# Kernel optimization log

Hardware: AMD Instinct MI355X
Metric: run time of the kernel (lower is better)

Reference implementation:

```python
import jax, jax.numpy as jnp
import numpy as np

B, LQ, LK, E, HID, H = 4, 1024, 2048, 512, 512, 8


def _ln(x, g, b, eps=1e-5):
    mu = jnp.mean(x, -1, keepdims=True)
    var = jnp.mean((x - mu) ** 2, -1, keepdims=True)
    return (x - mu) * jax.lax.rsqrt(var + eps) * g + b


def _mha(q_in, k_in, v_in, Wq, bq, Wk, bk, Wv, bv, Wo, bo, nheads, q_valid, k_valid):
    # torch nn.MultiheadAttention (batch_first, eval/dropout=0) math
    Bq, Lq, Em = q_in.shape
    Lk = k_in.shape[1]
    hd = Em // nheads
    q = (q_in @ Wq.T + bq).reshape(Bq, Lq, nheads, hd)
    k = (k_in @ Wk.T + bk).reshape(Bq, Lk, nheads, hd)
    v = (v_in @ Wv.T + bv).reshape(Bq, Lk, nheads, hd)
    scale = 1.0 / np.sqrt(hd).astype(np.float32)
    s = jnp.einsum('bqhd,bkhd->bhqk', q, k) * scale
    if k_valid is not None:
        # valid query rows may only attend to valid key columns
        s = jnp.where(k_valid[:, None, None, :], s, jnp.finfo(s.dtype).min)
    w = jax.nn.softmax(s, axis=-1)
    # rows beyond a sample's length are fully masked in the torch nested path
    # (softmax -> NaN, later nan_to_num'd to 0); we zero them directly.
    w = jnp.where(q_valid[:, None, :, None], w, 0.0)
    o = jnp.einsum('bhqk,bkhd->bqhd', w, v).reshape(Bq, Lq, Em)
    return o @ Wo.T + bo, jnp.mean(w, axis=1)  # weights averaged over heads


def setup_inputs() -> dict:
    key = jax.random.key(0)
    ks = jax.random.split(key, 32)
    p = lambda i, shape: 0.02 * jax.random.normal(ks[i], shape, dtype=jnp.float32)
    inp = {
        'queries': jax.random.normal(ks[0], (B, LQ, E), dtype=jnp.float32),
        'keys': jax.random.normal(ks[1], (B, LK, E), dtype=jnp.float32),
        'q_len': jax.random.randint(ks[2], (B,), 1, LQ + 1),
        # cross-attention params
        'cWq': p(3, (E, E)), 'cbq': jnp.zeros((E,)),
        'cWk': p(4, (E, E)), 'cbk': jnp.zeros((E,)),
        'cWv': p(5, (E, E)), 'cbv': jnp.zeros((E,)),
        'cWo': p(6, (E, E)), 'cbo': jnp.zeros((E,)),
        # self-attention params
        'sWq': p(7, (HID, HID)), 'sbq': jnp.zeros((HID,)),
        'sWk': p(8, (HID, HID)), 'sbk': jnp.zeros((HID,)),
        'sWv': p(9, (HID, HID)), 'sbv': jnp.zeros((HID,)),
        'sWo': p(10, (HID, HID)), 'sbo': jnp.zeros((HID,)),
        # ffn + norms
        'Wf': p(11, (HID, E)), 'bf': jnp.zeros((HID,)),
        'g_cross': jnp.ones((E,)), 'b_cross': jnp.zeros((E,)),
        'g_ffn': jnp.ones((HID,)), 'b_ffn': jnp.zeros((HID,)),
        'g_self': jnp.ones((HID,)), 'b_self': jnp.zeros((HID,)),
    }
    return inp


def reference(queries, keys, q_len,
              cWq, cbq, cWk, cbk, cWv, cbv, cWo, cbo,
              sWq, sbq, sWk, sbk, sWv, sbv, sWo, sbo,
              Wf, bf, g_cross, b_cross, g_ffn, b_ffn, g_self, b_self):
    valid = jnp.arange(LQ)[None, :] < q_len[:, None]  # [B, LQ] ragged lengths
    q = jnp.where(valid[..., None], queries, 0.0)     # nested -> padded with 0
    # cross attention: valid rows attend to ALL keys (per the nested mask)
    cross, weights = _mha(q, keys, keys, cWq, cbq, cWk, cbk, cWv, cbv, cWo, cbo,
                          H, valid, None)
    q = _ln(jax.nn.silu(cross + q), g_cross, b_cross)
    f = q @ Wf.T + bf
    q = _ln(jax.nn.silu(q + f), g_ffn, b_ffn)  # q_dim == hidden_dim branch
    q = jnp.where(valid[..., None], q, 0.0)    # torch.nan_to_num on padded rows
    # self attention: valid rows attend only to valid rows of the same sample
    so, _ = _mha(q, q, q, sWq, sbq, sWk, sbk, sWv, sbv, sWo, sbo, H, valid, valid)
    q = _ln(jax.nn.silu(q + so), g_self, b_self)
    q = jnp.where(valid[..., None], q, 0.0)    # padded rows discarded by unbind
    return q, weights
```

## Files before the change

kernel.cpp:

```cpp
#include <hip/hip_runtime.h>

#define BB 4
#define SLQ 1024
#define SLK 2048
#define EE 512
#define HH 8
#define HD 64

typedef unsigned short u16;
typedef __attribute__((ext_vector_type(8))) short s16x8;
typedef __attribute__((ext_vector_type(4))) float f32x4;

__device__ __forceinline__ float bf2f(u16 u) {
  union { unsigned int i; float f; } v; v.i = ((unsigned int)u) << 16; return v.f;
}
__device__ __forceinline__ u16 f2bf(float f) {
  union { float f; unsigned int i; } v; v.f = f;
  unsigned int i = v.i;
  return (u16)((i + 0x7fffu + ((i >> 16) & 1u)) >> 16);
}

__device__ __forceinline__ void async16(const u16* g, u16* l) {
  __builtin_amdgcn_global_load_lds(
      (const __attribute__((address_space(1))) unsigned int*)g,
      (__attribute__((address_space(3))) unsigned int*)l, 16, 0, 0);
}

template<int BM, int BN, int MODE, int SKIPQ>
__global__ __launch_bounds__(256, (BM == 128 ? 4 : 6))
void gemm_nt(const u16* __restrict__ A, const u16* __restrict__ Bm,
             const float* __restrict__ bias, u16* __restrict__ C,
             int M, int N, int K, int lda, int ldb, int ldc,
             long sAz, long sBz, long sCz, float alpha, int Lsub,
             const int* __restrict__ qlen)
{
  constexpr int WTM = BM / 2, WTN = BN / 2;
  constexpr int MI = WTM / 16, NI = WTN / 16;
  constexpr int EPAD = WTN + 8;
  constexpr int SM1 = (BM + BN) * 32;
  constexpr int SM2 = (MODE == 0) ? 4 * WTM * EPAD : 0;
  constexpr int SM = (SM1 > SM2) ? SM1 : SM2;

  const int z = blockIdx.z;
  const int tileM = blockIdx.y * BM;
  const int tileN = blockIdx.x * BN;

  if (SKIPQ == 1) { if (tileM >= qlen[z >> 3]) return; }
  if (SKIPQ == 2) { int b = tileM >> 10; if ((tileM & 1023) >= qlen[b]) return; }

  __shared__ __align__(16) u16 smem[SM];
  u16* ldsA = smem;
  u16* ldsB = smem + BM * 32;

  const int t = threadIdx.x;
  const int lane = t & 63;
  const int wave = t >> 6;
  const int waveM = wave >> 1;
  const int waveN = wave & 1;
  const int lm = lane & 15;
  const int kg = lane >> 4;

  const u16* Ab = A + (long)z * sAz + (long)tileM * lda;
  const u16* Bb = Bm + (long)z * sBz + (long)tileN * ldb;

  f32x4 acc[MI][NI];
#pragma unroll
  for (int i = 0; i < MI; ++i)
#pragma unroll
    for (int j = 0; j < NI; ++j) acc[i][j] = (f32x4){0.f, 0.f, 0.f, 0.f};

  for (int kt = 0; kt < K; kt += 32) {
    __syncthreads();
#pragma unroll
    for (int i = 0; i < (BM * 4) / 256; ++i) {
      int c = i * 256 + t;
      async16(Ab + (long)(c >> 2) * lda + kt + (c & 3) * 8, ldsA + (c - lane) * 8);
    }
#pragma unroll
    for (int i = 0; i < (BN * 4) / 256; ++i) {
      int c = i * 256 + t;
      async16(Bb + (long)(c >> 2) * ldb + kt + (c & 3) * 8, ldsB + (c - lane) * 8);
    }
    __syncthreads();

    s16x8 aF[MI], bF[NI];
#pragma unroll
    for (int i = 0; i < MI; ++i)
      aF[i] = *(const s16x8*)&ldsA[(waveM * WTM + i * 16 + lm) * 32 + kg * 8];
#pragma unroll
    for (int j = 0; j < NI; ++j)
      bF[j] = *(const s16x8*)&ldsB[(waveN * WTN + j * 16 + lm) * 32 + kg * 8];
#pragma unroll
    for (int i = 0; i < MI; ++i)
#pragma unroll
      for (int j = 0; j < NI; ++j)
        acc[i][j] = __builtin_amdgcn_mfma_f32_16x16x32_bf16(aF[i], bF[j], acc[i][j], 0, 0, 0);
  }

  if (MODE == 0) {
    u16* ep = smem + wave * (WTM * EPAD);
    __syncthreads();
#pragma unroll
    for (int i = 0; i < MI; ++i)
#pragma unroll
      for (int j = 0; j < NI; ++j) {
        int n = waveN * WTN + j * 16 + lm;
        float bv = bias ? bias[tileN + n] : 0.0f;
#pragma unroll
        for (int r = 0; r < 4; ++r)
          ep[(i * 16 + kg * 4 + r) * EPAD + j * 16 + lm] = f2bf(acc[i][j][r] * alpha + bv);
      }
    const long Crow = (long)z * sCz + (long)(tileM + waveM * WTM) * ldc + tileN + waveN * WTN;
#pragma unroll
    for (int it = 0; it < (WTM * WTN) / 512; ++it) {
      int idx = it * 64 + lane;
      int row = idx / (WTN / 8), seg = idx % (WTN / 8);
      *(uint4*)&C[Crow + (long)row * ldc + seg * 8] =
          *(const uint4*)&ep[row * EPAD + seg * 8];
    }
  } else {
#pragma unroll
    for (int j = 0; j < NI; ++j) {
      int n = tileN + waveN * WTN + j * 16 + lm;
      float bv = bias ? bias[n] : 0.0f;
#pragma unroll
      for (int i = 0; i < MI; ++i) {
#pragma unroll
        for (int r = 0; r < 4; ++r) {
          int m = tileM + waveM * WTM + i * 16 + kg * 4 + r;
          float v = acc[i][j][r] * alpha + bv;
          int b = m / Lsub, l = m - b * Lsub;
          int h = n >> 6, d = n & 63;
          C[(((long)(b * HH + h) * Lsub + l) << 6) + d] = f2bf(v);
        }
      }
    }
  }
}

template<int BM, int BN, int SKIPQ, int NPROJ>
__global__ __launch_bounds__(256, 6)
void gemm_proj(const u16* __restrict__ A,
               const u16* B0, const u16* B1, const u16* B2,
               const float* bias0, const float* bias1, const float* bias2,
               u16* C0, u16* C1, u16* C2,
               int M, int lda, int Lsub, const int* __restrict__ qlen)
{
  constexpr int WTM = BM / 2, WTN = BN / 2;
  constexpr int MI = WTM / 16, NI = WTN / 16;

  const int z = blockIdx.z;
  const int tileM = blockIdx.y * BM;
  const int tileN = blockIdx.x * BN;
  if (SKIPQ == 2) { int b = tileM >> 10; if ((tileM & 1023) >= qlen[b]) return; }

  const u16* Bm = (z == 0) ? B0 : (z == 1) ? B1 : B2;
  const float* bias = (z == 0) ? bias0 : (z == 1) ? bias1 : bias2;
  u16* C = (z == 0) ? C0 : (z == 1) ? C1 : C2;
  const bool tr = (z == NPROJ - 1);

  __shared__ __align__(16) u16 smem[(BM + BN) * 32];
  u16* ldsA = smem;
  u16* ldsB = smem + BM * 32;

  const int t = threadIdx.x;
  const int lane = t & 63;
  const int wave = t >> 6;
  const int waveM = wave >> 1;
  const int waveN = wave & 1;
  const int lm = lane & 15;
  const int kg = lane >> 4;

  const u16* Ab = A + (long)tileM * lda;
  const u16* Bb = Bm + (long)tileN * EE;

  f32x4 acc[MI][NI];
#pragma unroll
  for (int i = 0; i < MI; ++i)
#pragma unroll
    for (int j = 0; j < NI; ++j) acc[i][j] = (f32x4){0.f, 0.f, 0.f, 0.f};

  for (int kt = 0; kt < EE; kt += 32) {
    __syncthreads();
#pragma unroll
    for (int i = 0; i < (BM * 4) / 256; ++i) {
      int c = i * 256 + t;
      async16(Ab + (long)(c >> 2) * lda + kt + (c & 3) * 8, ldsA + (c - lane) * 8);
    }
#pragma unroll
    for (int i = 0; i < (BN * 4) / 256; ++i) {
      int c = i * 256 + t;
      async16(Bb + (long)(c >> 2) * EE + kt + (c & 3) * 8, ldsB + (c - lane) * 8);
    }
    __syncthreads();

    s16x8 aF[MI], bF[NI];
#pragma unroll
    for (int i = 0; i < MI; ++i)
      aF[i] = *(const s16x8*)&ldsA[(waveM * WTM + i * 16 + lm) * 32 + kg * 8];
#pragma unroll
    for (int j = 0; j < NI; ++j)
      bF[j] = *(const s16x8*)&ldsB[(waveN * WTN + j * 16 + lm) * 32 + kg * 8];
#pragma unroll
    for (int i = 0; i < MI; ++i)
#pragma unroll
      for (int j = 0; j < NI; ++j)
        acc[i][j] = __builtin_amdgcn_mfma_f32_16x16x32_bf16(aF[i], bF[j], acc[i][j], 0, 0, 0);
  }

  if (!tr) {
#pragma unroll
    for (int j = 0; j < NI; ++j) {
      int n = tileN + waveN * WTN + j * 16 + lm;
      float bv = bias[n];
#pragma unroll
      for (int i = 0; i < MI; ++i)
#pragma unroll
        for (int r = 0; r < 4; ++r) {
          int m = tileM + waveM * WTM + i * 16 + kg * 4 + r;
          int b = m / Lsub, l = m - b * Lsub;
          int h = n >> 6, d = n & 63;
          C[(((long)(b * HH + h) * Lsub + l) << 6) + d] = f2bf(acc[i][j][r] + bv);
        }
    }
  } else {
    constexpr int PAD = BM + 8;
    const int bb = tileM / Lsub;
    const int l0 = tileM - bb * Lsub;
#pragma unroll
    for (int c = 0; c < BN / 32; ++c) {
      __syncthreads();
#pragma unroll
      for (int j = 0; j < NI; ++j) {
        int nloc = waveN * WTN + j * 16 + lm;
        if (nloc >= c * 32 && nloc < c * 32 + 32) {
          int nl = nloc - c * 32;
          float bv = bias[tileN + nloc];
#pragma unroll
          for (int i = 0; i < MI; ++i)
#pragma unroll
            for (int r = 0; r < 4; ++r) {
              int mm = waveM * WTM + i * 16 + kg * 4 + r;
              smem[nl * PAD + mm] = f2bf(acc[i][j][r] + bv);
            }
        }
      }
      __syncthreads();
#pragma unroll
      for (int v = 0; v < (32 * BM) / (256 * 8); ++v) {
        int idx = v * 256 + t;
        int nl = idx / (BM / 8), m8 = idx % (BM / 8);
        int n = tileN + c * 32 + nl;
        int h = n >> 6, d = n & 63;
        *(uint4*)&C[((long)(bb * HH + h) * HD + d) * Lsub + l0 + m8 * 8] =
            *(const uint4*)&smem[nl * PAD + m8 * 8];
      }
    }
  }
}

__global__ __launch_bounds__(256, 3)
void cross_flash_chunk(const u16* __restrict__ Qc, const u16* __restrict__ Kc,
                       const u16* __restrict__ Vt, u16* __restrict__ Opart,
                       float2* __restrict__ ml, const int* __restrict__ qlen)
{
  const int qt = blockIdx.x;
  const int bh = blockIdx.y;
  const int ck = blockIdx.z;
  const int b = bh >> 3;
  if (qt * 64 >= qlen[b]) return;

  __shared__ __align__(16) u16 Kt[128 * 72];
  __shared__ __align__(16) u16 Vl[64 * 136];
  __shared__ __align__(16) u16 Pl[4 * 16 * 136];

  const int t = threadIdx.x, lane = t & 63, w = t >> 6;
  const int col = lane & 15, quad = lane >> 4;

  const u16* Qb = Qc + (long)bh * SLQ * HD;
  const u16* Kb = Kc + (long)bh * SLK * HD;
  const u16* Vb = Vt + (long)bh * HD * SLK;

  s16x8 aQ[2];
#pragma unroll
  for (int kk = 0; kk < 2; ++kk)
    aQ[kk] = *(const s16x8*)(Qb + (long)(qt * 64 + w * 16 + col) * HD + kk * 32 + quad * 8);

  f32x4 O[4];
  float mr[4], lr[4];
#pragma unroll
  for (int n = 0; n < 4; ++n) O[n] = (f32x4){0.f, 0.f, 0.f, 0.f};
#pragma unroll
  for (int r = 0; r < 4; ++r) { mr[r] = -1e30f; lr[r] = 0.f; }

  u16* Pw = Pl + w * 16 * 136;

  for (int kt = 0; kt < 4; ++kt) {
    const int k0 = ck * 512 + kt * 128;
    __syncthreads();
    for (int c = t; c < 1024; c += 256) {
      int r = c >> 3, c8 = c & 7;
      *(uint4*)&Kt[r * 72 + c8 * 8] = *(const uint4*)(Kb + (long)(k0 + r) * HD + c8 * 8);
    }
    for (int c = t; c < 1024; c += 256) {
      int d = c >> 4, c16 = c & 15;
      *(uint4*)&Vl[d * 136 + c16 * 8] = *(const uint4*)(Vb + (long)d * SLK + k0 + c16 * 8);
    }
    __syncthreads();

    f32x4 s[8];
#pragma unroll
    for (int j = 0; j < 8; ++j) s[j] = (f32x4){0.f, 0.f, 0.f, 0.f};
#pragma unroll
    for (int j = 0; j < 8; ++j)
#pragma unroll
      for (int kk = 0; kk < 2; ++kk) {
        s16x8 bK = *(const s16x8*)&Kt[(j * 16 + col) * 72 + kk * 32 + quad * 8];
        s[j] = __builtin_amdgcn_mfma_f32_16x16x32_bf16(aQ[kk], bK, s[j], 0, 0, 0);
      }
#pragma unroll
    for (int j = 0; j < 8; ++j)
#pragma unroll
      for (int r = 0; r < 4; ++r)
        s[j][r] *= 0.125f;
#pragma unroll
    for (int r = 0; r < 4; ++r) {
      float tm = s[0][r];
#pragma unroll
      for (int j = 1; j < 8; ++j) tm = fmaxf(tm, s[j][r]);
#pragma unroll
      for (int o = 1; o <= 8; o <<= 1) tm = fmaxf(tm, __shfl_xor(tm, o));
      float mnew = fmaxf(mr[r], tm);
      float alpha = __expf(mr[r] - mnew);
      mr[r] = mnew;
      float ps = 0.f;
#pragma unroll
      for (int j = 0; j < 8; ++j) {
        float p = __expf(s[j][r] - mnew);
        s[j][r] = p;
        ps += p;
      }
#pragma unroll
      for (int o = 1; o <= 8; o <<= 1) ps += __shfl_xor(ps, o);
      lr[r] = lr[r] * alpha + ps;
#pragma unroll
      for (int n = 0; n < 4; ++n) O[n][r] *= alpha;
    }
#pragma unroll
    for (int j = 0; j < 8; ++j)
#pragma unroll
      for (int r = 0; r < 4; ++r)
        Pw[(quad * 4 + r) * 136 + j * 16 + col] = f2bf(s[j][r]);
#pragma unroll
    for (int kk = 0; kk < 4; ++kk) {
      s16x8 aP = *(const s16x8*)&Pw[col * 136 + kk * 32 + quad * 8];
#pragma unroll
      for (int n = 0; n < 4; ++n) {
        s16x8 bV = *(const s16x8*)&Vl[(n * 16 + col) * 136 + kk * 32 + quad * 8];
        O[n] = __builtin_amdgcn_mfma_f32_16x16x32_bf16(aP, bV, O[n], 0, 0, 0);
      }
    }
  }

#pragma unroll
  for (int r = 0; r < 4; ++r) {
    int q = qt * 64 + w * 16 + quad * 4 + r;
    long gq = (long)bh * SLQ + q;
#pragma unroll
    for (int n = 0; n < 4; ++n)
      Opart[(gq * 4 + ck) * 64 + n * 16 + col] = f2bf(O[n][r]);
    if (col == 0) ml[gq * 4 + ck] = (float2){mr[r], lr[r]};
  }
}

__global__ __launch_bounds__(256)
void cross_combine(const u16* __restrict__ Opart, const float2* __restrict__ ml,
                   u16* __restrict__ attn, float2* __restrict__ stat,
                   const int* __restrict__ qlen)
{
  int gr = blockIdx.x * 16 + (threadIdx.x >> 4);
  int bh = gr >> 10, q = gr & 1023;
  int b = bh >> 3, h = bh & 7;
  if (q >= qlen[b]) return;
  int d = (threadIdx.x & 15) * 4;
  long base = (long)gr * 4;
  float M = -1e30f;
#pragma unroll
  for (int c = 0; c < 4; ++c) M = fmaxf(M, ml[base + c].x);
  float L = 0.f;
  float ax = 0.f, ay = 0.f, az = 0.f, aw = 0.f;
#pragma unroll
  for (int c = 0; c < 4; ++c) {
    float2 st = ml[base + c];
    float wgt = __expf(st.x - M);
    L += st.y * wgt;
    const u16* p = Opart + (base + c) * 64 + d;
    ax += bf2f(p[0]) * wgt; ay += bf2f(p[1]) * wgt;
    az += bf2f(p[2]) * wgt; aw += bf2f(p[3]) * wgt;
  }
  if (d == 0) stat[gr] = (float2){M, L};
  float inv = 1.0f / L;
  unsigned int lo = (unsigned int)f2bf(ax * inv) | ((unsigned int)f2bf(ay * inv) << 16);
  unsigned int hi = (unsigned int)f2bf(az * inv) | ((unsigned int)f2bf(aw * inv) << 16);
  *(uint2*)&attn[((long)b * SLQ + q) * EE + h * HD + d] = (uint2){lo, hi};
}

__global__ __launch_bounds__(256, 4)
void wmean_recompute(const u16* __restrict__ Qc, const u16* __restrict__ Kc,
                     const float2* __restrict__ stat, float* __restrict__ outw,
                     const int* __restrict__ qlen)
{
  const int kt = blockIdx.x;
  const int qt = blockIdx.y;
  const int b  = blockIdx.z;
  const int qn = qlen[b];
  const int q0 = qt * 64;
  const int t = threadIdx.x, lane = t & 63, w = t >> 6;
  const int col = lane & 15, quad = lane >> 4;

  float* wr = outw + ((long)b * SLQ + q0) * SLK + kt * 128;

  if (q0 >= qn) {
    float4 z = {0.f, 0.f, 0.f, 0.f};
    for (int i = t; i < 64 * 32; i += 256) {
      int row = i >> 5, c = (i & 31) << 2;
      *(float4*)&wr[(long)row * SLK + c] = z;
    }
    return;
  }

  __shared__ __align__(16) u16 Kl[128 * 72];

  const int qw = q0 + w * 16;
  const u16* Kbase = Kc + ((long)b * HH * SLK + (long)kt * 128) * HD;

  uint4 kreg[4];
#pragma unroll
  for (int i = 0; i < 4; ++i) {
    int c = i * 256 + t;
    kreg[i] = *(const uint4*)(Kbase + (long)(c >> 3) * HD + (c & 7) * 8);
  }

  f32x4 acc[8];
#pragma unroll
  for (int j = 0; j < 8; ++j) acc[j] = (f32x4){0.f, 0.f, 0.f, 0.f};

#pragma unroll 1
  for (int h = 0; h < 8; ++h) {
    const int bh = b * 8 + h;
    __syncthreads();
#pragma unroll
    for (int i = 0; i < 4; ++i) {
      int c = i * 256 + t;
      *(uint4*)&Kl[(c >> 3) * 72 + (c & 7) * 8] = kreg[i];
    }
    if (h < 7) {
      const u16* Kn = Kbase + (long)(h + 1) * SLK * HD;
#pragma unroll
      for (int i = 0; i < 4; ++i) {
        int c = i * 256 + t;
        kreg[i] = *(const uint4*)(Kn + (long)(c >> 3) * HD + (c & 7) * 8);
      }
    }
    const u16* Qb = Qc + ((long)bh * SLQ + qw) * HD;
    s16x8 aQ0 = *(const s16x8*)(Qb + col * HD + quad * 8);
    s16x8 aQ1 = *(const s16x8*)(Qb + col * HD + 32 + quad * 8);
    float m_[4], il_[4];
#pragma unroll
    for (int r = 0; r < 4; ++r) {
      float2 st = stat[(long)bh * SLQ + qw + quad * 4 + r];
      m_[r] = st.x; il_[r] = 0.125f / st.y;
    }
    __syncthreads();

    f32x4 s[8];
#pragma unroll
    for (int j = 0; j < 8; ++j) s[j] = (f32x4){0.f, 0.f, 0.f, 0.f};
#pragma unroll
    for (int j = 0; j < 8; ++j) {
      s16x8 bK0 = *(const s16x8*)&Kl[(j * 16 + col) * 72 + quad * 8];
      s16x8 bK1 = *(const s16x8*)&Kl[(j * 16 + col) * 72 + 32 + quad * 8];
      s[j] = __builtin_amdgcn_mfma_f32_16x16x32_bf16(aQ0, bK0, s[j], 0, 0, 0);
      s[j] = __builtin_amdgcn_mfma_f32_16x16x32_bf16(aQ1, bK1, s[j], 0, 0, 0);
    }
#pragma unroll
    for (int j = 0; j < 8; ++j)
#pragma unroll
      for (int r = 0; r < 4; ++r)
        acc[j][r] += __expf(s[j][r] * 0.125f - m_[r]) * il_[r];
  }

#pragma unroll
  for (int r = 0; r < 4; ++r) {
    int row = w * 16 + quad * 4 + r;
    bool v = (q0 + row) < qn;
#pragma unroll
    for (int j = 0; j < 8; ++j)
      wr[(long)row * SLK + j * 16 + col] = v ? acc[j][r] : 0.f;
  }
}

__global__ __launch_bounds__(256, 3)
void self_flash_chunk(const u16* __restrict__ Qc, const u16* __restrict__ Kc,
                      const u16* __restrict__ Vt, u16* __restrict__ Opart,
                      float2* __restrict__ ml, const int* __restrict__ qlen)
{
  const int qt = blockIdx.x;
  const int bh = blockIdx.y;
  const int ck = blockIdx.z;
  const int b = bh >> 3;
  const int kmax = qlen[b];
  if (qt * 64 >= kmax || ck * 256 >= kmax) return;

  __shared__ __align__(16) u16 Kt[128 * 72];
  __shared__ __align__(16) u16 Vl[64 * 136];
  __shared__ __align__(16) u16 Pl[4 * 16 * 136];

  const int t = threadIdx.x, lane = t & 63, w = t >> 6;
  const int col = lane & 15, quad = lane >> 4;

  const u16* Qb = Qc + (long)bh * SLQ * HD;
  const u16* Kb = Kc + (long)bh * SLQ * HD;
  const u16* Vb = Vt + (long)bh * HD * SLQ;

  s16x8 aQ[2];
#pragma unroll
  for (int kk = 0; kk < 2; ++kk)
    aQ[kk] = *(const s16x8*)(Qb + (long)(qt * 64 + w * 16 + col) * HD + kk * 32 + quad * 8);

  f32x4 O[4];
  float mr[4], lr[4];
#pragma unroll
  for (int n = 0; n < 4; ++n) O[n] = (f32x4){0.f, 0.f, 0.f, 0.f};
#pragma unroll
  for (int r = 0; r < 4; ++r) { mr[r] = -1e30f; lr[r] = 0.f; }

  u16* Pw = Pl + w * 16 * 136;

  for (int kt = 0; kt < 2; ++kt) {
    const int k0 = ck * 256 + kt * 128;
    if (k0 >= kmax) break;
    __syncthreads();
    for (int c = t; c < 1024; c += 256) {
      int r = c >> 3, c8 = c & 7;
      *(uint4*)&Kt[r * 72 + c8 * 8] = *(const uint4*)(Kb + (long)(k0 + r) * HD + c8 * 8);
    }
    for (int c = t; c < 1024; c += 256) {
      int d = c >> 4, c16 = c & 15;
      *(uint4*)&Vl[d * 136 + c16 * 8] = *(const uint4*)(Vb + (long)d * SLQ + k0 + c16 * 8);
    }
    __syncthreads();

    f32x4 s[8];
#pragma unroll
    for (int j = 0; j < 8; ++j) s[j] = (f32x4){0.f, 0.f, 0.f, 0.f};
#pragma unroll
    for (int j = 0; j < 8; ++j)
#pragma unroll
      for (int kk = 0; kk < 2; ++kk) {
        s16x8 bK = *(const s16x8*)&Kt[(j * 16 + col) * 72 + kk * 32 + quad * 8];
        s[j] = __builtin_amdgcn_mfma_f32_16x16x32_bf16(aQ[kk], bK, s[j], 0, 0, 0);
      }
#pragma unroll
    for (int j = 0; j < 8; ++j) {
      bool ok = (k0 + j * 16 + col) < kmax;
#pragma unroll
      for (int r = 0; r < 4; ++r)
        s[j][r] = ok ? s[j][r] * 0.125f : -1e30f;
    }
#pragma unroll
    for (int r = 0; r < 4; ++r) {
      float tm = s[0][r];
#pragma unroll
      for (int j = 1; j < 8; ++j) tm = fmaxf(tm, s[j][r]);
#pragma unroll
      for (int o = 1; o <= 8; o <<= 1) tm = fmaxf(tm, __shfl_xor(tm, o));
      float mnew = fmaxf(mr[r], tm);
      float alpha = __expf(mr[r] - mnew);
      mr[r] = mnew;
      float ps = 0.f;
#pragma unroll
      for (int j = 0; j < 8; ++j) {
        float p = __expf(s[j][r] - mnew);
        s[j][r] = p;
        ps += p;
      }
#pragma unroll
      for (int o = 1; o <= 8; o <<= 1) ps += __shfl_xor(ps, o);
      lr[r] = lr[r] * alpha + ps;
#pragma unroll
      for (int n = 0; n < 4; ++n) O[n][r] *= alpha;
    }
#pragma unroll
    for (int j = 0; j < 8; ++j)
#pragma unroll
      for (int r = 0; r < 4; ++r)
        Pw[(quad * 4 + r) * 136 + j * 16 + col] = f2bf(s[j][r]);
#pragma unroll
    for (int kk = 0; kk < 4; ++kk) {
      s16x8 aP = *(const s16x8*)&Pw[col * 136 + kk * 32 + quad * 8];
#pragma unroll
      for (int n = 0; n < 4; ++n) {
        s16x8 bV = *(const s16x8*)&Vl[(n * 16 + col) * 136 + kk * 32 + quad * 8];
        O[n] = __builtin_amdgcn_mfma_f32_16x16x32_bf16(aP, bV, O[n], 0, 0, 0);
      }
    }
  }

#pragma unroll
  for (int r = 0; r < 4; ++r) {
    int q = qt * 64 + w * 16 + quad * 4 + r;
    long gq = (long)bh * SLQ + q;
#pragma unroll
    for (int n = 0; n < 4; ++n)
      Opart[(gq * 4 + ck) * 64 + n * 16 + col] = f2bf(O[n][r]);
    if (col == 0) ml[gq * 4 + ck] = (float2){mr[r], lr[r]};
  }
}

__global__ __launch_bounds__(256)
void self_combine(const u16* __restrict__ Opart, const float2* __restrict__ ml,
                  u16* __restrict__ attn, const int* __restrict__ qlen)
{
  int gr = blockIdx.x * 16 + (threadIdx.x >> 4);
  int bh = gr >> 10, q = gr & 1023;
  int b = bh >> 3, h = bh & 7;
  int kmax = qlen[b];
  if (q >= kmax) return;
  int NC = (kmax + 255) >> 8;
  int d = (threadIdx.x & 15) * 4;
  long base = (long)gr * 4;
  float M = -1e30f;
  for (int c = 0; c < NC; ++c) M = fmaxf(M, ml[base + c].x);
  float L = 0.f;
  float ax = 0.f, ay = 0.f, az = 0.f, aw = 0.f;
  for (int c = 0; c < NC; ++c) {
    float2 st = ml[base + c];
    float wgt = __expf(st.x - M);
    L += st.y * wgt;
    const u16* p = Opart + (base + c) * 64 + d;
    ax += bf2f(p[0]) * wgt; ay += bf2f(p[1]) * wgt;
    az += bf2f(p[2]) * wgt; aw += bf2f(p[3]) * wgt;
  }
  float inv = 1.0f / L;
  unsigned int lo = (unsigned int)f2bf(ax * inv) | ((unsigned int)f2bf(ay * inv) << 16);
  unsigned int hi = (unsigned int)f2bf(az * inv) | ((unsigned int)f2bf(aw * inv) << 16);
  *(uint2*)&attn[((long)b * SLQ + q) * EE + h * HD + d] = (uint2){lo, hi};
}

__global__ __launch_bounds__(256)
void cvt_all(const float* __restrict__ queries, const float* __restrict__ keys,
             const int* __restrict__ qlen,
             const float* w0, const float* w1, const float* w2, const float* w3,
             const float* w4, const float* w5, const float* w6, const float* w7,
             const float* w8,
             u16* __restrict__ q0, u16* __restrict__ keysb, u16* __restrict__ Wb) {
  int blk = blockIdx.x;
  int t = threadIdx.x;
  const float* src;
  u16* dst;
  long off;
  bool mask = false;
  int b = 0, q = 0;
  if (blk < 1024) {
    off = (long)blk * 2048 + t * 8;
    int row = (int)(off >> 9);
    b = row >> 10; q = row & 1023;
    mask = true;
    src = queries; dst = q0;
  } else if (blk < 3072) {
    off = (long)(blk - 1024) * 2048 + t * 8;
    src = keys; dst = keysb;
  } else {
    int mat = (blk - 3072) >> 7, part = (blk - 3072) & 127;
    const float* srcs[9] = {w0, w1, w2, w3, w4, w5, w6, w7, w8};
    src = srcs[mat];
    off = (long)part * 2048 + t * 8;
    dst = Wb + (long)mat * EE * EE;
  }
  s16x8 o = (s16x8){0, 0, 0, 0, 0, 0, 0, 0};
  if (!mask || q < qlen[b]) {
    float4 a = *(const float4*)&src[off];
    float4 c = *(const float4*)&src[off + 4];
    o[0] = (short)f2bf(a.x); o[1] = (short)f2bf(a.y);
    o[2] = (short)f2bf(a.z); o[3] = (short)f2bf(a.w);
    o[4] = (short)f2bf(c.x); o[5] = (short)f2bf(c.y);
    o[6] = (short)f2bf(c.z); o[7] = (short)f2bf(c.w);
  }
  *(s16x8*)&dst[off] = o;
}

__device__ __forceinline__ float blockSum(float v, float* red4) {
#pragma unroll
  for (int o = 32; o; o >>= 1) v += __shfl_xor(v, o);
  if ((threadIdx.x & 63) == 0) red4[threadIdx.x >> 6] = v;
  __syncthreads();
  v = red4[0] + red4[1] + red4[2] + red4[3];
  __syncthreads();
  return v;
}

template<int OUTF32>
__global__ __launch_bounds__(256)
void silu_ln_kernel(const u16* __restrict__ x1, const u16* __restrict__ x2,
                    const float* __restrict__ g, const float* __restrict__ beta,
                    const int* __restrict__ qlen, void* __restrict__ outv, int mode) {
  int row = blockIdx.x;
  int b = row >> 10, q = row & 1023;
  int t = threadIdx.x;
  if (mode && q >= qlen[b]) {
    if (mode == 1) {
      if (OUTF32) {
        float* o = (float*)outv + (long)row * EE;
        o[2 * t] = 0.f; o[2 * t + 1] = 0.f;
      } else {
        u16* o = (u16*)outv + (long)row * EE;
        *(unsigned int*)&o[2 * t] = 0u;
      }
    }
    return;
  }
  __shared__ float red4[4];
  const u16* p1 = x1 + (long)row * EE;
  const u16* p2 = x2 + (long)row * EE;
  float a0 = bf2f(p1[2 * t]) + bf2f(p2[2 * t]);
  float a1 = bf2f(p1[2 * t + 1]) + bf2f(p2[2 * t + 1]);
  a0 = a0 / (1.f + __expf(-a0));
  a1 = a1 / (1.f + __expf(-a1));
  float mu = blockSum(a0 + a1, red4) * (1.f / 512.f);
  float d0 = a0 - mu, d1 = a1 - mu;
  float var = blockSum(d0 * d0 + d1 * d1, red4) * (1.f / 512.f);
  float rs = rsqrtf(var + 1e-5f);
  float r0 = d0 * rs * g[2 * t] + beta[2 * t];
  float r1 = d1 * rs * g[2 * t + 1] + beta[2 * t + 1];
  if (OUTF32) {
    float* o = (float*)outv + (long)row * EE;
    o[2 * t] = r0; o[2 * t + 1] = r1;
  } else {
    u16* o = (u16*)outv + (long)row * EE;
    o[2 * t] = f2bf(r0); o[2 * t + 1] = f2bf(r1);
  }
}

extern "C" void kernel_launch(void* const* d_in, const int* in_sizes, int n_in,
                              void* d_out, int out_size, void* d_ws, size_t ws_size,
                              hipStream_t stream) {
  const float* queries = (const float*)d_in[0];
  const float* keys    = (const float*)d_in[1];
  const int*   qlen    = (const int*)d_in[2];
  const float* cWq = (const float*)d_in[3],  *cbq = (const float*)d_in[4];
  const float* cWk = (const float*)d_in[5],  *cbk = (const float*)d_in[6];
  const float* cWv = (const float*)d_in[7],  *cbv = (const float*)d_in[8];
  const float* cWo = (const float*)d_in[9],  *cbo = (const float*)d_in[10];
  const float* sWq = (const float*)d_in[11], *sbq = (const float*)d_in[12];
  const float* sWk = (const float*)d_in[13], *sbk = (const float*)d_in[14];
  const float* sWv = (const float*)d_in[15], *sbv = (const float*)d_in[16];
  const float* sWo = (const float*)d_in[17], *sbo = (const float*)d_in[18];
  const float* Wf  = (const float*)d_in[19], *bfb = (const float*)d_in[20];
  const float* g_cross = (const float*)d_in[21], *b_cross = (const float*)d_in[22];
  const float* g_ffn   = (const float*)d_in[23], *b_ffn   = (const float*)d_in[24];
  const float* g_self  = (const float*)d_in[25], *b_self  = (const float*)d_in[26];

  float* out_q = (float*)d_out;
  float* out_w = out_q + (long)BB * SLQ * EE;

  u16* ws = (u16*)d_ws;
  u16* S     = ws;
  u16* Qc    = S   + (long)BB * HH * SLQ * SLK;
  u16* Kc    = Qc  + (long)BB * HH * SLQ * HD;
  u16* Vt    = Kc  + (long)BB * HH * SLK * HD;
  u16* q0    = Vt  + (long)BB * HH * SLK * HD;
  u16* keysb = q0  + (long)BB * SLQ * EE;
  u16* attn  = keysb + (long)BB * SLK * EE;
  u16* proj  = attn + (long)BB * SLQ * EE;
  u16* q1    = proj + (long)BB * SLQ * EE;
  u16* fbuf  = q1  + (long)BB * SLQ * EE;
  u16* q2    = fbuf + (long)BB * SLQ * EE;
  u16* Wb    = q2  + (long)BB * SLQ * EE;
  const long WSLOT = (long)EE * EE;
  u16*    Cpb  = Wb + 9 * WSLOT;
  float2* stat = (float2*)(Cpb + 8388608);

  float2* mlC = (float2*)(S + 33554432);

  u16*    OpS = S;
  float2* mlS = (float2*)(S + 8388608);

  u16* bWq = Wb + 0 * WSLOT; u16* bWk = Wb + 1 * WSLOT; u16* bWv = Wb + 2 * WSLOT;
  u16* bWo = Wb + 3 * WSLOT; u16* bsWq = Wb + 4 * WSLOT; u16* bsWk = Wb + 5 * WSLOT;
  u16* bsWv = Wb + 6 * WSLOT; u16* bsWo = Wb + 7 * WSLOT; u16* bWf = Wb + 8 * WSLOT;

  dim3 blk(256);
  const int MQ = BB * SLQ;
  const int MK = BB * SLK;

  cvt_all<<<dim3(3072 + 9 * 128), blk, 0, stream>>>(
      queries, keys, qlen, cWq, cWk, cWv, cWo, sWq, sWk, sWv, sWo, Wf, q0, keysb, Wb);

  gemm_nt<64, 64, 1, 2><<<dim3(EE / 64, MQ / 64, 1), blk, 0, stream>>>(
      q0, bWq, cbq, Qc, MQ, EE, EE, EE, EE, 0, 0, 0, 0, 1.0f, SLQ, qlen);
  gemm_proj<64, 64, 0, 2><<<dim3(EE / 64, MK / 64, 2), blk, 0, stream>>>(
      keysb, bWk, bWv, nullptr, cbk, cbv, nullptr, Kc, Vt, nullptr, MK, EE, SLK, qlen);

  cross_flash_chunk<<<dim3(16, 32, 4), blk, 0, stream>>>(Qc, Kc, Vt, Cpb, mlC, qlen);
  cross_combine<<<dim3(2048), blk, 0, stream>>>(Cpb, mlC, attn, stat, qlen);
  wmean_recompute<<<dim3(16, 16, BB), blk, 0, stream>>>(Qc, Kc, stat, out_w, qlen);

  gemm_nt<64, 64, 0, 2><<<dim3(EE / 64, MQ / 64, 1), blk, 0, stream>>>(
      attn, bWo, cbo, proj, MQ, EE, EE, EE, EE, EE, 0, 0, 0, 1.0f, SLQ, qlen);

  silu_ln_kernel<0><<<dim3(MQ), blk, 0, stream>>>(proj, q0, g_cross, b_cross, qlen, q1, 2);

  gemm_nt<64, 64, 0, 2><<<dim3(EE / 64, MQ / 64, 1), blk, 0, stream>>>(
      q1, bWf, bfb, fbuf, MQ, EE, EE, EE, EE, EE, 0, 0, 0, 1.0f, SLQ, qlen);

  silu_ln_kernel<0><<<dim3(MQ), blk, 0, stream>>>(q1, fbuf, g_ffn, b_ffn, qlen, q2, 1);

  gemm_proj<64, 64, 2, 3><<<dim3(EE / 64, MQ / 64, 3), blk, 0, stream>>>(
      q2, bsWq, bsWk, bsWv, sbq, sbk, sbv, Qc, Kc, Vt, MQ, EE, SLQ, qlen);

  self_flash_chunk<<<dim3(16, 32, 4), blk, 0, stream>>>(Qc, Kc, Vt, OpS, mlS, qlen);
  self_combine<<<dim3(2048), blk, 0, stream>>>(OpS, mlS, attn, qlen);

  gemm_nt<64, 64, 0, 2><<<dim3(EE / 64, MQ / 64, 1), blk, 0, stream>>>(
      attn, bsWo, sbo, proj, MQ, EE, EE, EE, EE, EE, 0, 0, 0, 1.0f, SLQ, qlen);

  silu_ln_kernel<1><<<dim3(MQ), blk, 0, stream>>>(q2, proj, g_self, b_self, qlen, out_q, 1);
}
```

Before: 358.6 us.

## Prefetch next K/V tile into registers and remap flash blocks across XCDs

Both flash-attention chunk kernels now load the next 128-key K and V tile into registers while the current tile is being computed, then write it to shared memory at the start of the next iteration. This is meant to hide global memory latency behind the MFMA and softmax work. The 3D grid is also flattened to 1D with a block-index swizzle (lin&7 selects a group of 256), so that neighbouring work lands on the same XCD for L2 reuse. The cost is extra VGPRs for the eight uint4 staging registers, which may hurt occupancy at launch bounds of 3 blocks per CU.

New measurement: 380.4 us. 6.1% more time.

```diff
diff --git a/kernel.cpp b/kernel.cpp
--- a/kernel.cpp
+++ b/kernel.cpp
@@ -264,9 +264,11 @@
                        const u16* __restrict__ Vt, u16* __restrict__ Opart,
                        float2* __restrict__ ml, const int* __restrict__ qlen)
 {
-  const int qt = blockIdx.x;
-  const int bh = blockIdx.y;
-  const int ck = blockIdx.z;
+  const int lin = blockIdx.x;
+  const int lid = (lin & 7) * 256 + (lin >> 3);
+  const int qt = lid & 15;
+  const int bh = (lid >> 4) & 31;
+  const int ck = lid >> 9;
   const int b = bh >> 3;
   if (qt * 64 >= qlen[b]) return;
 
@@ -295,16 +297,45 @@
 
   u16* Pw = Pl + w * 16 * 136;
 
+  uint4 kreg[4], vreg[4];
+  {
+    const int k0 = ck * 512;
+#pragma unroll
+    for (int i = 0; i < 4; ++i) {
+      int c = i * 256 + t;
+      kreg[i] = *(const uint4*)(Kb + (long)(k0 + (c >> 3)) * HD + (c & 7) * 8);
+    }
+#pragma unroll
+    for (int i = 0; i < 4; ++i) {
+      int c = i * 256 + t;
+      vreg[i] = *(const uint4*)(Vb + (long)(c >> 4) * SLK + k0 + (c & 15) * 8);
+    }
+  }
+
   for (int kt = 0; kt < 4; ++kt) {
-    const int k0 = ck * 512 + kt * 128;
-    __syncthreads();
-    for (int c = t; c < 1024; c += 256) {
-      int r = c >> 3, c8 = c & 7;
-      *(uint4*)&Kt[r * 72 + c8 * 8] = *(const uint4*)(Kb + (long)(k0 + r) * HD + c8 * 8);
-    }
-    for (int c = t; c < 1024; c += 256) {
-      int d = c >> 4, c16 = c & 15;
-      *(uint4*)&Vl[d * 136 + c16 * 8] = *(const uint4*)(Vb + (long)d * SLK + k0 + c16 * 8);
+    __syncthreads();
+#pragma unroll
+    for (int i = 0; i < 4; ++i) {
+      int c = i * 256 + t;
+      *(uint4*)&Kt[(c >> 3) * 72 + (c & 7) * 8] = kreg[i];
+    }
+#pragma unroll
+    for (int i = 0; i < 4; ++i) {
+      int c = i * 256 + t;
+      *(uint4*)&Vl[(c >> 4) * 136 + (c & 15) * 8] = vreg[i];
+    }
+    if (kt < 3) {
+      const int k1 = ck * 512 + (kt + 1) * 128;
+#pragma unroll
+      for (int i = 0; i < 4; ++i) {
+        int c = i * 256 + t;
+        kreg[i] = *(const uint4*)(Kb + (long)(k1 + (c >> 3)) * HD + (c & 7) * 8);
+      }
+#pragma unroll
+      for (int i = 0; i < 4; ++i) {
+        int c = i * 256 + t;
+        vreg[i] = *(const uint4*)(Vb + (long)(c >> 4) * SLK + k1 + (c & 15) * 8);
+      }
     }
     __syncthreads();
 
@@ -505,9 +536,11 @@
                       const u16* __restrict__ Vt, u16* __restrict__ Opart,
                       float2* __restrict__ ml, const int* __restrict__ qlen)
 {
-  const int qt = blockIdx.x;
-  const int bh = blockIdx.y;
-  const int ck = blockIdx.z;
+  const int lin = blockIdx.x;
+  const int lid = (lin & 7) * 256 + (lin >> 3);
+  const int qt = lid & 15;
+  const int bh = (lid >> 4) & 31;
+  const int ck = lid >> 9;
   const int b = bh >> 3;
   const int kmax = qlen[b];
   if (qt * 64 >= kmax || ck * 256 >= kmax) return;
@@ -537,17 +570,47 @@
 
   u16* Pw = Pl + w * 16 * 136;
 
+  uint4 kreg[4], vreg[4];
+  {
+    const int k0 = ck * 256;
+#pragma unroll
+    for (int i = 0; i < 4; ++i) {
+      int c = i * 256 + t;
+      kreg[i] = *(const uint4*)(Kb + (long)(k0 + (c >> 3)) * HD + (c & 7) * 8);
+    }
+#pragma unroll
+    for (int i = 0; i < 4; ++i) {
+      int c = i * 256 + t;
+      vreg[i] = *(const uint4*)(Vb + (long)(c >> 4) * SLQ + k0 + (c & 15) * 8);
+    }
+  }
+
   for (int kt = 0; kt < 2; ++kt) {
     const int k0 = ck * 256 + kt * 128;
     if (k0 >= kmax) break;
     __syncthreads();
-    for (int c = t; c < 1024; c += 256) {
-      int r = c >> 3, c8 = c & 7;
-      *(uint4*)&Kt[r * 72 + c8 * 8] = *(const uint4*)(Kb + (long)(k0 + r) * HD + c8 * 8);
-    }
-    for (int c = t; c < 1024; c += 256) {
-      int d = c >> 4, c16 = c & 15;
-      *(uint4*)&Vl[d * 136 + c16 * 8] = *(const uint4*)(Vb + (long)d * SLQ + k0 + c16 * 8);
+#pragma unroll
+    for (int i = 0; i < 4; ++i) {
+      int c = i * 256 + t;
+      *(uint4*)&Kt[(c >> 3) * 72 + (c & 7) * 8] = kreg[i];
+    }
+#pragma unroll
+    for (int i = 0; i < 4; ++i) {
+      int c = i * 256 + t;
+      *(uint4*)&Vl[(c >> 4) * 136 + (c & 15) * 8] = vreg[i];
+    }
+    if (kt < 1) {
+      const int k1 = ck * 256 + 128;
+#pragma unroll
+      for (int i = 0; i < 4; ++i) {
+        int c = i * 256 + t;
+        kreg[i] = *(const uint4*)(Kb + (long)(k1 + (c >> 3)) * HD + (c & 7) * 8);
+      }
+#pragma unroll
+      for (int i = 0; i < 4; ++i) {
+        int c = i * 256 + t;
+        vreg[i] = *(const uint4*)(Vb + (long)(c >> 4) * SLQ + k1 + (c & 15) * 8);
+      }
     }
     __syncthreads();
 
@@ -802,7 +865,7 @@
   gemm_proj<64, 64, 0, 2><<<dim3(EE / 64, MK / 64, 2), blk, 0, stream>>>(
       keysb, bWk, bWv, nullptr, cbk, cbv, nullptr, Kc, Vt, nullptr, MK, EE, SLK, qlen);
 
-  cross_flash_chunk<<<dim3(16, 32, 4), blk, 0, stream>>>(Qc, Kc, Vt, Cpb, mlC, qlen);
+  cross_flash_chunk<<<dim3(2048), blk, 0, stream>>>(Qc, Kc, Vt, Cpb, mlC, qlen);
   cross_combine<<<dim3(2048), blk, 0, stream>>>(Cpb, mlC, attn, stat, qlen);
   wmean_recompute<<<dim3(16, 16, BB), blk, 0, stream>>>(Qc, Kc, stat, out_w, qlen);
 
@@ -819,7 +882,7 @@
   gemm_proj<64, 64, 2, 3><<<dim3(EE / 64, MQ / 64, 3), blk, 0, stream>>>(
       q2, bsWq, bsWk, bsWv, sbq, sbk, sbv, Qc, Kc, Vt, MQ, EE, SLQ, qlen);
 
-  self_flash_chunk<<<dim3(16, 32, 4), blk, 0, stream>>>(Qc, Kc, Vt, OpS, mlS, qlen);
+  self_flash_chunk<<<dim3(2048), blk, 0, stream>>>(Qc, Kc, Vt, OpS, mlS, qlen);
   self_combine<<<dim3(2048), blk, 0, stream>>>(OpS, mlS, attn, qlen);
 
   gemm_nt<64, 64, 0, 2><<<dim3(EE / 64, MQ / 64, 1), blk, 0, stream>>>(
```

## Register-prefetch next K/V tiles and remap flash block order for XCD locality

Applied to the files above, without the earlier changes.

The cross and self flash-attention kernels now load the next 128-key K and V tiles into registers while the current tile is being processed, rather than issuing synchronous global loads right before each LDS store. Both kernels also move to a 1D grid whose block index is permuted (lin&7 selects a group), so consecutive blocks dispatched round-robin across the eight XCDs map to neighbouring (q-tile, head, chunk) work and share K/V in each XCD's L2. The wmean kernel's prefetch loop is unrolled by hand. The aim is to hide global-load latency and improve cache reuse, at the cost of more live registers, which could hurt occupancy under the 3-blocks launch bound.

Measured after the change: 307.5 us. 1.17x faster.

```diff
diff --git a/kernel.cpp b/kernel.cpp
--- a/kernel.cpp
+++ b/kernel.cpp
@@ -264,9 +264,11 @@
                        const u16* __restrict__ Vt, u16* __restrict__ Opart,
                        float2* __restrict__ ml, const int* __restrict__ qlen)
 {
-  const int qt = blockIdx.x;
-  const int bh = blockIdx.y;
-  const int ck = blockIdx.z;
+  const int lin = blockIdx.x;
+  const int lid = (lin & 7) * 256 + (lin >> 3);
+  const int qt = lid & 15;
+  const int bh = (lid >> 4) & 31;
+  const int ck = lid >> 9;
   const int b = bh >> 3;
   if (qt * 64 >= qlen[b]) return;
 
@@ -295,16 +297,43 @@
 
   u16* Pw = Pl + w * 16 * 136;
 
+  const int krow = t >> 3, kcol = (t & 7) * 8;
+  const int vrow = t >> 4, vcol = (t & 15) * 8;
+
+  uint4 kr0, kr1, kr2, kr3, vr0, vr1, vr2, vr3;
+  {
+    const int kb = ck * 512;
+    kr0 = *(const uint4*)(Kb + (long)(kb + krow) * HD + kcol);
+    kr1 = *(const uint4*)(Kb + (long)(kb + krow + 32) * HD + kcol);
+    kr2 = *(const uint4*)(Kb + (long)(kb + krow + 64) * HD + kcol);
+    kr3 = *(const uint4*)(Kb + (long)(kb + krow + 96) * HD + kcol);
+    vr0 = *(const uint4*)(Vb + (long)(vrow) * SLK + kb + vcol);
+    vr1 = *(const uint4*)(Vb + (long)(vrow + 16) * SLK + kb + vcol);
+    vr2 = *(const uint4*)(Vb + (long)(vrow + 32) * SLK + kb + vcol);
+    vr3 = *(const uint4*)(Vb + (long)(vrow + 48) * SLK + kb + vcol);
+  }
+
+#pragma unroll
   for (int kt = 0; kt < 4; ++kt) {
-    const int k0 = ck * 512 + kt * 128;
-    __syncthreads();
-    for (int c = t; c < 1024; c += 256) {
-      int r = c >> 3, c8 = c & 7;
-      *(uint4*)&Kt[r * 72 + c8 * 8] = *(const uint4*)(Kb + (long)(k0 + r) * HD + c8 * 8);
-    }
-    for (int c = t; c < 1024; c += 256) {
-      int d = c >> 4, c16 = c & 15;
-      *(uint4*)&Vl[d * 136 + c16 * 8] = *(const uint4*)(Vb + (long)d * SLK + k0 + c16 * 8);
+    __syncthreads();
+    *(uint4*)&Kt[(krow) * 72 + kcol] = kr0;
+    *(uint4*)&Kt[(krow + 32) * 72 + kcol] = kr1;
+    *(uint4*)&Kt[(krow + 64) * 72 + kcol] = kr2;
+    *(uint4*)&Kt[(krow + 96) * 72 + kcol] = kr3;
+    *(uint4*)&Vl[(vrow) * 136 + vcol] = vr0;
+    *(uint4*)&Vl[(vrow + 16) * 136 + vcol] = vr1;
+    *(uint4*)&Vl[(vrow + 32) * 136 + vcol] = vr2;
+    *(uint4*)&Vl[(vrow + 48) * 136 + vcol] = vr3;
+    if (kt < 3) {
+      const int kb = ck * 512 + (kt + 1) * 128;
+      kr0 = *(const uint4*)(Kb + (long)(kb + krow) * HD + kcol);
+      kr1 = *(const uint4*)(Kb + (long)(kb + krow + 32) * HD + kcol);
+      kr2 = *(const uint4*)(Kb + (long)(kb + krow + 64) * HD + kcol);
+      kr3 = *(const uint4*)(Kb + (long)(kb + krow + 96) * HD + kcol);
+      vr0 = *(const uint4*)(Vb + (long)(vrow) * SLK + kb + vcol);
+      vr1 = *(const uint4*)(Vb + (long)(vrow + 16) * SLK + kb + vcol);
+      vr2 = *(const uint4*)(Vb + (long)(vrow + 32) * SLK + kb + vcol);
+      vr3 = *(const uint4*)(Vb + (long)(vrow + 48) * SLK + kb + vcol);
     }
     __syncthreads();
 
@@ -434,12 +463,13 @@
   const int qw = q0 + w * 16;
   const u16* Kbase = Kc + ((long)b * HH * SLK + (long)kt * 128) * HD;
 
-  uint4 kreg[4];
-#pragma unroll
-  for (int i = 0; i < 4; ++i) {
-    int c = i * 256 + t;
-    kreg[i] = *(const uint4*)(Kbase + (long)(c >> 3) * HD + (c & 7) * 8);
-  }
+  const int krow = t >> 3, kcol = (t & 7) * 8;
+
+  uint4 kr0, kr1, kr2, kr3;
+  kr0 = *(const uint4*)(Kbase + (long)(krow) * HD + kcol);
+  kr1 = *(const uint4*)(Kbase + (long)(krow + 32) * HD + kcol);
+  kr2 = *(const uint4*)(Kbase + (long)(krow + 64) * HD + kcol);
+  kr3 = *(const uint4*)(Kbase + (long)(krow + 96) * HD + kcol);
 
   f32x4 acc[8];
 #pragma unroll
@@ -449,18 +479,16 @@
   for (int h = 0; h < 8; ++h) {
     const int bh = b * 8 + h;
     __syncthreads();
-#pragma unroll
-    for (int i = 0; i < 4; ++i) {
-      int c = i * 256 + t;
-      *(uint4*)&Kl[(c >> 3) * 72 + (c & 7) * 8] = kreg[i];
-    }
+    *(uint4*)&Kl[(krow) * 72 + kcol] = kr0;
+    *(uint4*)&Kl[(krow + 32) * 72 + kcol] = kr1;
+    *(uint4*)&Kl[(krow + 64) * 72 + kcol] = kr2;
+    *(uint4*)&Kl[(krow + 96) * 72 + kcol] = kr3;
     if (h < 7) {
       const u16* Kn = Kbase + (long)(h + 1) * SLK * HD;
-#pragma unroll
-      for (int i = 0; i < 4; ++i) {
-        int c = i * 256 + t;
-        kreg[i] = *(const uint4*)(Kn + (long)(c >> 3) * HD + (c & 7) * 8);
-      }
+      kr0 = *(const uint4*)(Kn + (long)(krow) * HD + kcol);
+      kr1 = *(const uint4*)(Kn + (long)(krow + 32) * HD + kcol);
+      kr2 = *(const uint4*)(Kn + (long)(krow + 64) * HD + kcol);
+      kr3 = *(const uint4*)(Kn + (long)(krow + 96) * HD + kcol);
     }
     const u16* Qb = Qc + ((long)bh * SLQ + qw) * HD;
     s16x8 aQ0 = *(const s16x8*)(Qb + col * HD + quad * 8);
@@ -505,9 +533,11 @@
                       const u16* __restrict__ Vt, u16* __restrict__ Opart,
                       float2* __restrict__ ml, const int* __restrict__ qlen)
 {
-  const int qt = blockIdx.x;
-  const int bh = blockIdx.y;
-  const int ck = blockIdx.z;
+  const int lin = blockIdx.x;
+  const int lid = (lin & 7) * 256 + (lin >> 3);
+  const int qt = lid & 15;
+  const int bh = (lid >> 4) & 31;
+  const int ck = lid >> 9;
   const int b = bh >> 3;
   const int kmax = qlen[b];
   if (qt * 64 >= kmax || ck * 256 >= kmax) return;
@@ -537,17 +567,45 @@
 
   u16* Pw = Pl + w * 16 * 136;
 
+  const int krow = t >> 3, kcol = (t & 7) * 8;
+  const int vrow = t >> 4, vcol = (t & 15) * 8;
+
+  uint4 kr0, kr1, kr2, kr3, vr0, vr1, vr2, vr3;
+  {
+    const int kb = ck * 256;
+    kr0 = *(const uint4*)(Kb + (long)(kb + krow) * HD + kcol);
+    kr1 = *(const uint4*)(Kb + (long)(kb + krow + 32) * HD + kcol);
+    kr2 = *(const uint4*)(Kb + (long)(kb + krow + 64) * HD + kcol);
+    kr3 = *(const uint4*)(Kb + (long)(kb + krow + 96) * HD + kcol);
+    vr0 = *(const uint4*)(Vb + (long)(vrow) * SLQ + kb + vcol);
+    vr1 = *(const uint4*)(Vb + (long)(vrow + 16) * SLQ + kb + vcol);
+    vr2 = *(const uint4*)(Vb + (long)(vrow + 32) * SLQ + kb + vcol);
+    vr3 = *(const uint4*)(Vb + (long)(vrow + 48) * SLQ + kb + vcol);
+  }
+
+#pragma unroll
   for (int kt = 0; kt < 2; ++kt) {
     const int k0 = ck * 256 + kt * 128;
     if (k0 >= kmax) break;
     __syncthreads();
-    for (int c = t; c < 1024; c += 256) {
-      int r = c >> 3, c8 = c & 7;
-      *(uint4*)&Kt[r * 72 + c8 * 8] = *(const uint4*)(Kb + (long)(k0 + r) * HD + c8 * 8);
-    }
-    for (int c = t; c < 1024; c += 256) {
-      int d = c >> 4, c16 = c & 15;
-      *(uint4*)&Vl[d * 136 + c16 * 8] = *(const uint4*)(Vb + (long)d * SLQ + k0 + c16 * 8);
+    *(uint4*)&Kt[(krow) * 72 + kcol] = kr0;
+    *(uint4*)&Kt[(krow + 32) * 72 + kcol] = kr1;
+    *(uint4*)&Kt[(krow + 64) * 72 + kcol] = kr2;
+    *(uint4*)&Kt[(krow + 96) * 72 + kcol] = kr3;
+    *(uint4*)&Vl[(vrow) * 136 + vcol] = vr0;
+    *(uint4*)&Vl[(vrow + 16) * 136 + vcol] = vr1;
+    *(uint4*)&Vl[(vrow + 32) * 136 + vcol] = vr2;
+    *(uint4*)&Vl[(vrow + 48) * 136 + vcol] = vr3;
+    if (kt < 1) {
+      const int kb = ck * 256 + 128;
+      kr0 = *(const uint4*)(Kb + (long)(kb + krow) * HD + kcol);
+      kr1 = *(const uint4*)(Kb + (long)(kb + krow + 32) * HD + kcol);
+      kr2 = *(const uint4*)(Kb + (long)(kb + krow + 64) * HD + kcol);
+      kr3 = *(const uint4*)(Kb + (long)(kb + krow + 96) * HD + kcol);
+      vr0 = *(const uint4*)(Vb + (long)(vrow) * SLQ + kb + vcol);
+      vr1 = *(const uint4*)(Vb + (long)(vrow + 16) * SLQ + kb + vcol);
+      vr2 = *(const uint4*)(Vb + (long)(vrow + 32) * SLQ + kb + vcol);
+      vr3 = *(const uint4*)(Vb + (long)(vrow + 48) * SLQ + kb + vcol);
     }
     __syncthreads();
 
@@ -802,7 +860,7 @@
   gemm_proj<64, 64, 0, 2><<<dim3(EE / 64, MK / 64, 2), blk, 0, stream>>>(
       keysb, bWk, bWv, nullptr, cbk, cbv, nullptr, Kc, Vt, nullptr, MK, EE, SLK, qlen);
 
-  cross_flash_chunk<<<dim3(16, 32, 4), blk, 0, stream>>>(Qc, Kc, Vt, Cpb, mlC, qlen);
+  cross_flash_chunk<<<dim3(2048), blk, 0, stream>>>(Qc, Kc, Vt, Cpb, mlC, qlen);
   cross_combine<<<dim3(2048), blk, 0, stream>>>(Cpb, mlC, attn, stat, qlen);
   wmean_recompute<<<dim3(16, 16, BB), blk, 0, stream>>>(Qc, Kc, stat, out_w, qlen);
 
@@ -819,7 +877,7 @@
   gemm_proj<64, 64, 2, 3><<<dim3(EE / 64, MQ / 64, 3), blk, 0, stream>>>(
       q2, bsWq, bsWk, bsWv, sbq, sbk, sbv, Qc, Kc, Vt, MQ, EE, SLQ, qlen);
 
-  self_flash_chunk<<<dim3(16, 32, 4), blk, 0, stream>>>(Qc, Kc, Vt, OpS, mlS, qlen);
+  self_flash_chunk<<<dim3(2048), blk, 0, stream>>>(Qc, Kc, Vt, OpS, mlS, qlen);
   self_combine<<<dim3(2048), blk, 0, stream>>>(OpS, mlS, attn, qlen);
 
   gemm_nt<64, 64, 0, 2><<<dim3(EE / 64, MQ / 64, 1), blk, 0, stream>>>(
```
